# Performance work log

Hardware: AMD Instinct MI355X
Metric: run time of the kernel (lower is better)

Reference implementation:

```python
import jax, jax.numpy as jnp
import numpy as np

B, Cin, Cout, H, W = 8, 64, 128, 64, 64
DI, N, R, K = 256, 16, 8, 4  # d_inner, d_state, dt_rank, scan directions
EPS = 1e-5


def setup_inputs() -> dict:
    key = jax.random.key(0)
    ks = jax.random.split(key, 12)
    rn = lambda k, s, sc=1.0: jax.random.normal(k, s, jnp.float32) * sc
    inp = {
        "x": rn(ks[0], (B, Cin, H, W)),
        "conv1_w": rn(ks[1], (Cout, Cin, 3, 3), 0.05),
        "bn1_g": jnp.ones((Cout,)), "bn1_b": jnp.zeros((Cout,)),
        "bn1_m": jnp.zeros((Cout,)), "bn1_v": jnp.ones((Cout,)),
        "conv2_w": rn(ks[2], (Cout, Cout, 3, 3), 0.05),
        "bn2_g": jnp.ones((Cout,)), "bn2_b": jnp.zeros((Cout,)),
        "bn2_m": jnp.zeros((Cout,)), "bn2_v": jnp.ones((Cout,)),
        "ln_g": jnp.ones((Cout,)), "ln_b": jnp.zeros((Cout,)),
        "in_proj_w": rn(ks[3], (2 * DI, Cout), 0.05),
        "in_proj_b": jnp.zeros((2 * DI,)),
        "dw_w": rn(ks[4], (DI, 1, 3, 3), 0.2),
        "dw_b": jnp.zeros((DI,)),
        "x_proj_w": rn(ks[5], (K, R + 2 * N, DI), 0.05),
        "dt_proj_w": rn(ks[6], (K, DI, R), 0.1),
        "dt_proj_b": rn(ks[7], (K, DI), 0.1),
        "A_log": jnp.log(jnp.broadcast_to(jnp.arange(1, N + 1, dtype=jnp.float32), (K, DI, N))),
        "Ds": jnp.ones((K, DI)),
        "out_norm_g": jnp.ones((DI,)), "out_norm_b": jnp.zeros((DI,)),
        "out_proj_w": rn(ks[8], (Cout, DI), 0.05),
        "out_proj_b": jnp.zeros((Cout,)),
    }
    return inp


def _conv(x, w, groups=1):
    return jax.lax.conv_general_dilated(x, w, (1, 1), 'SAME',
        dimension_numbers=('NCHW', 'OIHW', 'NCHW'), feature_group_count=groups)


def _bn(x, g, b, m, v):
    inv = g / jnp.sqrt(v + EPS)
    return x * inv[:, None, None] + (b - m * inv)[:, None, None]


def _ln_cf(x, g, b):
    # LayerNorm over channel axis, channel-first [B,C,H,W]
    mu = x.mean(1, keepdims=True)
    var = ((x - mu) ** 2).mean(1, keepdims=True)
    return (x - mu) / jnp.sqrt(var + EPS) * g[None, :, None, None] + b[None, :, None, None]


def _selective_scan(u, dt, A, Bs, Cs, Ds):
    # u, dt: [B,K,D,L]; Bs, Cs: [B,K,N,L]; A: [K,D,N]; Ds: [K,D]
    uT = jnp.moveaxis(u, -1, 0)    # [L,B,K,D]
    dtT = jnp.moveaxis(dt, -1, 0)  # [L,B,K,D]
    BT = jnp.moveaxis(Bs, -1, 0)   # [L,B,K,N]
    CT = jnp.moveaxis(Cs, -1, 0)   # [L,B,K,N]

    def step(h, inp):
        u_i, dt_i, B_i, C_i = inp
        dA = jnp.exp(dt_i[..., None] * A)                       # [B,K,D,N]
        h = dA * h + (dt_i * u_i)[..., None] * B_i[:, :, None, :]
        y = jnp.einsum('bkdn,bkn->bkd', h, C_i)
        return h, y

    h0 = jnp.zeros(u.shape[:3] + (A.shape[-1],), u.dtype)       # [B,K,D,N]
    _, ys = jax.lax.scan(step, h0, (uT, dtT, BT, CT))
    ys = jnp.moveaxis(ys, 0, -1)                                # [B,K,D,L]
    return ys + u * Ds[None, :, :, None]


def _ss2d(x, ln_g, ln_b, in_proj_w, in_proj_b, dw_w, dw_b, x_proj_w,
          dt_proj_w, dt_proj_b, A_log, Ds, out_norm_g, out_norm_b,
          out_proj_w, out_proj_b):
    b, c, h, w = x.shape
    L = h * w
    xn = _ln_cf(x, ln_g, ln_b)
    xz = jnp.einsum('bchw,oc->bohw', xn, in_proj_w) + in_proj_b[None, :, None, None]
    xg, z = xz[:, :DI], xz[:, DI:]
    xc = jax.nn.silu(_conv(xg, dw_w, groups=DI) + dw_b[None, :, None, None])  # [B,DI,H,W]

    # cross-scan: 4 traversal orders of the 2D grid
    x_hw = xc.reshape(b, DI, L)
    x_wh = xc.transpose(0, 1, 3, 2).reshape(b, DI, L)
    xs = jnp.stack([x_hw, x_wh, jnp.flip(x_hw, -1), jnp.flip(x_wh, -1)], 1)  # [B,K,DI,L]

    x_dbl = jnp.einsum('bkdl,kcd->bkcl', xs, x_proj_w)
    dts, Bs, Cs = x_dbl[:, :, :R], x_dbl[:, :, R:R + N], x_dbl[:, :, R + N:]
    dt = jax.nn.softplus(jnp.einsum('bkrl,kdr->bkdl', dts, dt_proj_w)
                         + dt_proj_b[None, :, :, None])
    A = -jnp.exp(A_log)

    ys = _selective_scan(xs, dt, A, Bs, Cs, Ds)                 # [B,K,DI,L]

    # cross-merge: undo each traversal and sum
    y_wh = ys[:, 1] + jnp.flip(ys[:, 3], -1)
    y = ys[:, 0] + jnp.flip(ys[:, 2], -1) \
        + y_wh.reshape(b, DI, w, h).transpose(0, 1, 3, 2).reshape(b, DI, L)
    y = y.reshape(b, DI, h, w)

    y = _ln_cf(y, out_norm_g, out_norm_b)
    y = y * jax.nn.silu(z)
    return jnp.einsum('bdhw,od->bohw', y, out_proj_w) + out_proj_b[None, :, None, None]


def reference(x, conv1_w, bn1_g, bn1_b, bn1_m, bn1_v, conv2_w, bn2_g, bn2_b,
              bn2_m, bn2_v, ln_g, ln_b, in_proj_w, in_proj_b, dw_w, dw_b,
              x_proj_w, dt_proj_w, dt_proj_b, A_log, Ds, out_norm_g,
              out_norm_b, out_proj_w, out_proj_b):
    # CNN stem: conv-BN-ReLU x2 (eval mode; Dropout2d identity)
    hcnn = jax.nn.relu(_bn(_conv(x, conv1_w), bn1_g, bn1_b, bn1_m, bn1_v))
    hcnn = jax.nn.relu(_bn(_conv(hcnn, conv2_w), bn2_g, bn2_b, bn2_m, bn2_v))
    # VSSBlock: residual + SS2D(LN(x))
    out = hcnn + _ss2d(hcnn, ln_g, ln_b, in_proj_w, in_proj_b, dw_w, dw_b,
                       x_proj_w, dt_proj_w, dt_proj_b, A_log, Ds,
                       out_norm_g, out_norm_b, out_proj_w, out_proj_b)
    return out
```

## Files before the change

### kernel.cpp

```cpp
#include <hip/hip_runtime.h>
#include <hip/hip_bf16.h>
#include <math.h>

typedef __hip_bfloat16 bf16;
typedef float f32x4 __attribute__((ext_vector_type(4)));
typedef float f32x2 __attribute__((ext_vector_type(2)));
typedef short s8v   __attribute__((ext_vector_type(8)));

#define EPSV 1e-5f
#define C1c  64
#define C2c  128
#define Ls   4096
#define DIc  256
#define NCH  64
#define CHL  64
#define LOG2E 1.44269504f

#define CPAD 40
#define SM_CONVM_BYTES ((3*66*CPAD + 9*64*CPAD)*2)
#define SM_PROJ2_BYTES ((192*CPAD + 64*CPAD)*2)
#define SM_SCAN   (32*40)
#define SM_NORM_BYTES (64*266*2 + 512*4)
#define SM_OUT_BYTES  ((64*CPAD + 128*CPAD)*2)

template<bool BF>
__device__ __forceinline__ float LD(const void* p, size_t i){
  if constexpr(BF) return __bfloat162float(((const bf16*)p)[i]);
  else return ((const float*)p)[i];
}

__device__ __forceinline__ int smap(int k, int l){
  if(k==0) return l;
  if(k==1) return ((l&63)<<6) | (l>>6);
  if(k==2) return 4095 - l;
  int lp = 4095 - l; return ((lp&63)<<6) | (lp>>6);
}

__device__ __forceinline__ float* sbase(float* S1, float* S2, int bid){
  return (bid & 1024) ? (S2 + ((size_t)(bid & 1023) << 12))
                      : (S1 + ((size_t)bid << 12));
}

__global__ void k_flag(const unsigned int* __restrict__ g1, int* __restrict__ fl){
  if(threadIdx.x==0 && blockIdx.x==0) *fl = (g1[0]==0x3F800000u) ? 0 : 1;
}

template<bool BF>
__device__ void wprep_impl(const void* w1, const void* w2, const void* w3, const void* w4s,
    const void* w5s, bf16* W1P, bf16* W2P, bf16* W3P, bf16* W4P, bf16* W5P){
  int idx = blockIdx.x*256 + threadIdx.x;
  if(idx < 9*128*64){
    int kk = idx>>13; int rem = idx&8191; int co = rem>>6; int ci = rem&63;
    W1P[idx] = __float2bfloat16(LD<BF>(w1, ((size_t)co*64+ci)*9 + kk));
  } else if(idx < 9*128*64 + 9*128*128){
    int i2 = idx - 9*128*64;
    int kk = i2>>14; int rem = i2&16383; int co = rem>>7; int ci = rem&127;
    W2P[i2] = __float2bfloat16(LD<BF>(w2, ((size_t)co*128+ci)*9 + kk));
  } else if(idx < 9*128*64 + 9*128*128 + 128*256){
    int i3 = idx - (9*128*64 + 9*128*128);
    W3P[i3] = __float2bfloat16(LD<BF>(w3, i3));
  } else if(idx < 9*128*64 + 9*128*128 + 128*256 + 512*128){
    int i4 = idx - (9*128*64 + 9*128*128 + 128*256);
    W4P[i4] = __float2bfloat16(LD<BF>(w4s, i4));
  } else if(idx < 9*128*64 + 9*128*128 + 128*256 + 512*128 + 4*48*256){
    int i5 = idx - (9*128*64 + 9*128*128 + 128*256 + 512*128);
    int k5 = i5/12288; int rem = i5 - k5*12288;
    int m = rem>>8; int c = rem&255;
    float v = (m < 40) ? LD<BF>(w5s, ((size_t)(k5*40+m))*256 + c) : 0.f;
    W5P[i5] = __float2bfloat16(v);
  }
}
__global__ __launch_bounds__(256) void k_wprep(const int* fl, const void* w1, const void* w2,
    const void* w3, const void* w4s, const void* w5s,
    bf16* W1P, bf16* W2P, bf16* W3P, bf16* W4P, bf16* W5P){
  if(*fl) wprep_impl<true>(w1,w2,w3,w4s,w5s,W1P,W2P,W3P,W4P,W5P);
  else    wprep_impl<false>(w1,w2,w3,w4s,w5s,W1P,W2P,W3P,W4P,W5P);
}

template<bool BF>
__device__ void xprep_impl(float* tile, const void* x, bf16* XT){
  int bid = blockIdx.x; int sc = bid & 63; int b = bid>>6;
  int t = threadIdx.x;
  #pragma unroll
  for(int i=0;i<16;i++){
    int flat = t + 256*i;
    int ci = flat>>6, px = flat&63;
    tile[ci*65+px] = LD<BF>(x, ((size_t)b*64+ci)*Ls + sc*64 + px);
  }
  __syncthreads();
  #pragma unroll
  for(int i=0;i<16;i++){
    int flat = t + 256*i;
    int px = flat>>6, ci = flat&63;
    XT[((size_t)b*Ls + sc*64 + px)*64 + ci] = __float2bfloat16(tile[ci*65+px]);
  }
}
__global__ __launch_bounds__(256) void k_xprep(const int* fl, const void* x, bf16* XT){
  __shared__ float tile[64*65];
  if(*fl) xprep_impl<true>(tile,x,XT); else xprep_impl<false>(tile,x,XT);
}

template<bool BFW, int CIN, bool OUTCL>
__device__ void convm2_impl(bf16* smb, const bf16* __restrict__ xt, const bf16* __restrict__ wp,
    const void* __restrict__ gg, const void* __restrict__ bbp, const void* __restrict__ mm,
    const void* __restrict__ vv, void* __restrict__ out){
  bf16* bx = smb;
  bf16* wl = smb + 3*66*CPAD;
  int bid = blockIdx.x;
  int y = bid & 63; int cog = (bid>>6)&1; int b = bid>>7;
  int t = threadIdx.x;
  int w = t>>6; int lane = t&63; int n = lane&15; int q = lane>>4;

  for(int i=t; i<3*66*CPAD/2; i+=256) ((unsigned int*)bx)[i] = 0u;

  f32x4 acc[4];
  #pragma unroll
  for(int pt=0;pt<4;pt++) acc[pt] = (f32x4){0.f,0.f,0.f,0.f};

  for(int ci0=0; ci0<CIN; ci0+=32){
    __syncthreads();
    #pragma unroll
    for(int i=0;i<3;i++){
      int idx = t + 256*i;
      int c8 = idx&3, px = (idx>>2)&63, r = idx>>8;
      int gy = y + r - 1;
      if((unsigned)gy < 64u){
        uint4 v = *(const uint4*)(xt + ((size_t)b*Ls + (gy<<6) + px)*CIN + ci0 + c8*8);
        *(uint4*)(bx + ((r*66) + px+1)*CPAD + c8*8) = v;
      }
    }
    #pragma unroll
    for(int i=0;i<9;i++){
      int idx = t + 256*i;
      int c8 = idx&3, co = (idx>>2)&63, kk = idx>>8;
      uint4 v = *(const uint4*)(wp + ((size_t)kk*128 + cog*64+co)*CIN + ci0 + c8*8);
      *(uint4*)(wl + (kk*64+co)*CPAD + c8*8) = v;
    }
    __syncthreads();
    #pragma unroll
    for(int kk=0; kk<9; kk++){
      int ky = kk/3, kx = kk - ky*3;
      s8v A = *(const s8v*)(wl + (kk*64 + w*16 + n)*CPAD + q*8);
      #pragma unroll
      for(int pt=0;pt<4;pt++){
        s8v B = *(const s8v*)(bx + (ky*66 + pt*16 + n + kx)*CPAD + q*8);
        acc[pt] = __builtin_amdgcn_mfma_f32_16x16x32_bf16(A, B, acc[pt], 0, 0, 0);
      }
    }
  }
  float inv[4], bias[4];
  #pragma unroll
  for(int i=0;i<4;i++){
    int co = cog*64 + w*16 + q*4 + i;
    float iv = LD<BFW>(gg,co)/sqrtf(LD<BFW>(vv,co)+EPSV);
    inv[i] = iv;
    bias[i] = LD<BFW>(bbp,co) - LD<BFW>(mm,co)*iv;
  }
  #pragma unroll
  for(int pt=0;pt<4;pt++){
    int px = pt*16 + n;
    if constexpr(OUTCL){
      ushort4 o4;
      unsigned short* ov = (unsigned short*)&o4;
      #pragma unroll
      for(int i=0;i<4;i++){
        float v = acc[pt][i]*inv[i] + bias[i];
        v = v>0.f ? v : 0.f;
        bf16 bv = __float2bfloat16(v);
        ov[i] = *(unsigned short*)&bv;
      }
      *(ushort4*)((bf16*)out + ((size_t)b*Ls + (y<<6) + px)*128 + cog*64 + w*16 + q*4) = o4;
    } else {
      #pragma unroll
      for(int i=0;i<4;i++){
        int co = cog*64 + w*16 + q*4 + i;
        float v = acc[pt][i]*inv[i] + bias[i];
        ((float*)out)[((size_t)b*C2c + co)*Ls + (y<<6) + px] = v>0.f ? v : 0.f;
      }
    }
  }
}
__global__ __launch_bounds__(256) void k_conv1(const int* fl, const bf16* xt, const bf16* wp,
    const void* g, const void* bb, const void* mm, const void* vv, bf16* out){
  extern __shared__ float sm[];
  bf16* smb = (bf16*)sm;
  if(*fl) convm2_impl<true ,C1c,true>(smb,xt,wp,g,bb,mm,vv,out);
  else    convm2_impl<false,C1c,true>(smb,xt,wp,g,bb,mm,vv,out);
}
__global__ __launch_bounds__(256) void k_conv2(const int* fl, const bf16* xt, const bf16* wp,
    const void* g, const void* bb, const void* mm, const void* vv, float* out){
  extern __shared__ float sm[];
  bf16* smb = (bf16*)sm;
  if(*fl) convm2_impl<true ,C2c,false>(smb,xt,wp,g,bb,mm,vv,out);
  else    convm2_impl<false,C2c,false>(smb,xt,wp,g,bb,mm,vv,out);
}

template<bool BF>
__device__ void ln1_impl(const float* __restrict__ hc, const void* __restrict__ g,
    const void* __restrict__ bb, float* __restrict__ xn){
  int t = threadIdx.x;
  int pos = blockIdx.x*64 + (t>>2);
  int part = t&3;
  int b = pos >> 12; int s = pos & 4095;
  const float* base = hc + (size_t)b*C2c*Ls + (size_t)(part*32)*Ls + s;
  float v[32];
  float sum=0.f, sq=0.f;
  #pragma unroll
  for(int j=0;j<32;j++){
    float x = base[(size_t)j*Ls];
    v[j] = x; sum += x; sq += x*x;
  }
  sum += __shfl_xor(sum,1); sum += __shfl_xor(sum,2);
  sq  += __shfl_xor(sq,1);  sq  += __shfl_xor(sq,2);
  float mu  = sum*(1.f/C2c);
  float var = sq*(1.f/C2c) - mu*mu;
  float inv = rsqrtf(var + EPSV);
  float* ob = xn + (size_t)b*C2c*Ls + (size_t)(part*32)*Ls + s;
  #pragma unroll
  for(int j=0;j<32;j++){
    int c = part*32 + j;
    ob[(size_t)j*Ls] = (v[j]-mu)*inv*LD<BF>(g,c) + LD<BF>(bb,c);
  }
}
__global__ __launch_bounds__(256) void k_ln1(const int* fl, const float* hc, const void* g,
    const void* bb, float* xn){
  if(*fl) ln1_impl<true>(hc,g,bb,xn); else ln1_impl<false>(hc,g,bb,xn);
}

template<bool BF>
__device__ void inprojm_impl(bf16* smb, const float* __restrict__ xn, const bf16* __restrict__ w4,
    const void* __restrict__ ipb, float* __restrict__ xg, float* __restrict__ sz){
  bf16* bm = smb;
  bf16* wl = smb + 64*CPAD;
  int bid = blockIdx.x;
  int y = bid & 63; int og = (bid>>6)&3; int b = bid>>8;
  int t = threadIdx.x;
  int w = t>>6; int lane = t&63; int n = lane&15; int q = lane>>4;
  f32x4 acc[2][4];
  #pragma unroll
  for(int si=0;si<2;si++)
    #pragma unroll
    for(int pt=0;pt<4;pt++) acc[si][pt] = (f32x4){0.f,0.f,0.f,0.f};
  for(int c0=0; c0<C2c; c0+=32){
    __syncthreads();
    #pragma unroll
    for(int i=0;i<2;i++){
      int task = t + 256*i;
      int px = task & 63; int cq = task >> 6;
      const float* src = xn + ((size_t)(b*C2c + c0 + cq*4))*Ls + (y<<6) + px;
      ushort4 o4;
      unsigned short* ov = (unsigned short*)&o4;
      #pragma unroll
      for(int r=0;r<4;r++){
        bf16 bv = __float2bfloat16(src[(size_t)r*Ls]);
        ov[r] = *(unsigned short*)&bv;
      }
      *(ushort4*)(bm + px*CPAD + cq*4) = o4;
    }
    #pragma unroll
    for(int i=0;i<2;i++){
      int idx = t + 256*i;
      int co = idx>>2, c8 = idx&3;
      *(uint4*)(wl + co*CPAD + c8*8) = *(const uint4*)(w4 + (size_t)(og*128+co)*C2c + c0 + c8*8);
    }
    __syncthreads();
    #pragma unroll
    for(int si=0;si<2;si++){
      s8v A = *(const s8v*)(wl + ((w*2+si)*16 + n)*CPAD + q*8);
      #pragma unroll
      for(int pt=0;pt<4;pt++){
        s8v B = *(const s8v*)(bm + (pt*16+n)*CPAD + q*8);
        acc[si][pt] = __builtin_amdgcn_mfma_f32_16x16x32_bf16(A, B, acc[si][pt], 0, 0, 0);
      }
    }
  }
  #pragma unroll
  for(int si=0;si<2;si++){
    #pragma unroll
    for(int i=0;i<4;i++){
      int o = og*128 + (w*2+si)*16 + q*4 + i;
      float bias = LD<BF>(ipb, o);
      #pragma unroll
      for(int pt=0;pt<4;pt++){
        int px = pt*16 + n;
        float v = acc[si][pt][i] + bias;
        size_t off = ((size_t)b*DIc + (o & 255))*Ls + (y<<6) + px;
        if(o < 256) xg[off] = v;
        else        sz[off] = v/(1.f+__expf(-v));
      }
    }
  }
}
__global__ __launch_bounds__(256) void k_inproj(const int* fl, const float* xn, const bf16* w4,
    const void* ipb, float* xg, float* sz){
  extern __shared__ float sm[];
  bf16* smb = (bf16*)sm;
  if(*fl) inprojm_impl<true>(smb,xn,w4,ipb,xg,sz); else inprojm_impl<false>(smb,xn,w4,ipb,xg,sz);
}

template<bool BF>
__device__ void dwconv_impl(const float* __restrict__ xg, const void* __restrict__ wt,
    const void* __restrict__ bias, float* __restrict__ xc){
  int bid = blockIdx.x;
  int st = bid & 15; int d = (bid>>4)&255; int b = bid>>12;
  int s = st*256 + threadIdx.x;
  int h = s>>6, w = s&63;
  const float* base = xg + ((size_t)b*DIc + d)*Ls;
  float acc = LD<BF>(bias, d);
  #pragma unroll
  for(int kh=0;kh<3;kh++){
    int hh = h+kh-1;
    if((unsigned)hh<64u){
      #pragma unroll
      for(int kw=0;kw<3;kw++){
        int ww = w+kw-1;
        if((unsigned)ww<64u) acc += base[(hh<<6)+ww]*LD<BF>(wt, d*9+kh*3+kw);
      }
    }
  }
  xc[((size_t)b*DIc+d)*Ls + s] = acc/(1.f+__expf(-acc));
}
__global__ __launch_bounds__(256) void k_dwconv(const int* fl, const float* xg, const void* wt,
    const void* bias, float* xc){
  if(*fl) dwconv_impl<true>(xg,wt,bias,xc); else dwconv_impl<false>(xg,wt,bias,xc);
}

__global__ __launch_bounds__(256) void k_trans(const float* __restrict__ xc, float* __restrict__ xcT){
  __shared__ float tile[64*65];
  int bid = blockIdx.x; int sc = bid & 63; int dc = (bid>>6)&3; int b = bid>>8;
  int s0 = sc*64, d0 = dc*64;
  int t = threadIdx.x;
  #pragma unroll
  for(int i=0;i<16;i++){
    int flat = t + 256*i;
    int dd = flat>>6, ss = flat&63;
    tile[dd*65+ss] = xc[((size_t)b*DIc + d0+dd)*Ls + s0+ss];
  }
  __syncthreads();
  #pragma unroll
  for(int i=0;i<16;i++){
    int flat = t + 256*i;
    int ss = flat>>6, dd = flat&63;
    xcT[((size_t)b*Ls + s0+ss)*DIc + d0+dd] = tile[dd*65+ss];
  }
}

__global__ __launch_bounds__(256) void k_proj2(const float* __restrict__ xcT,
    const bf16* __restrict__ w5, float* __restrict__ proj){
  extern __shared__ float smf[];
  bf16* wl = (bf16*)smf;
  bf16* bm = wl + 192*CPAD;
  int bid = blockIdx.x;
  int y = bid & 63; int b = bid>>6;
  int s0 = y*64;
  int t = threadIdx.x;
  int w = t>>6; int lane = t&63; int n = lane&15; int q = lane>>4;
  f32x4 acc[3][4];
  #pragma unroll
  for(int si=0;si<3;si++)
    #pragma unroll
    for(int pt=0;pt<4;pt++) acc[si][pt] = (f32x4){0.f,0.f,0.f,0.f};
  for(int c0=0; c0<DIc; c0+=32){
    __syncthreads();
    #pragma unroll
    for(int i=0;i<3;i++){
      int idx = t + 256*i;
      int co = idx>>2, c8 = idx&3;
      *(uint4*)(wl + co*CPAD + c8*8) = *(const uint4*)(w5 + (size_t)co*DIc + c0 + c8*8);
    }
    {
      int px = t & 63; int cq = t >> 6;
      const float* src = xcT + ((size_t)b*Ls + s0 + px)*DIc + c0 + cq*8;
      float4 v0 = *(const float4*)(src);
      float4 v1 = *(const float4*)(src+4);
      ushort4 o0, o1;
      unsigned short* p0 = (unsigned short*)&o0;
      unsigned short* p1 = (unsigned short*)&o1;
      const float* pv0 = (const float*)&v0;
      const float* pv1 = (const float*)&v1;
      #pragma unroll
      for(int r=0;r<4;r++){
        bf16 b0 = __float2bfloat16(pv0[r]); p0[r] = *(unsigned short*)&b0;
        bf16 b1 = __float2bfloat16(pv1[r]); p1[r] = *(unsigned short*)&b1;
      }
      *(ushort4*)(bm + px*CPAD + cq*8)     = o0;
      *(ushort4*)(bm + px*CPAD + cq*8 + 4) = o1;
    }
    __syncthreads();
    #pragma unroll
    for(int si=0;si<3;si++){
      s8v A = *(const s8v*)(wl + (w*48 + si*16 + n)*CPAD + q*8);
      #pragma unroll
      for(int pt=0;pt<4;pt++){
        s8v B = *(const s8v*)(bm + (pt*16+n)*CPAD + q*8);
        acc[si][pt] = __builtin_amdgcn_mfma_f32_16x16x32_bf16(A, B, acc[si][pt], 0, 0, 0);
      }
    }
  }
  float* ob = proj + (((size_t)b*4 + w)*Ls + s0)*40;
  #pragma unroll
  for(int si=0;si<3;si++){
    if(si==2 && q>=2) continue;
    int m0 = si*16 + q*4;
    #pragma unroll
    for(int pt=0;pt<4;pt++){
      int px = pt*16 + n;
      float4 v4; v4.x=acc[si][pt][0]; v4.y=acc[si][pt][1]; v4.z=acc[si][pt][2]; v4.w=acc[si][pt][3];
      *(float4*)(ob + (size_t)px*40 + m0) = v4;
    }
  }
}

template<bool BF>
__device__ void scanA_impl(float* lp, const float* __restrict__ xcT, const float* __restrict__ proj,
    const void* __restrict__ dtw_g, const void* __restrict__ dtb_g, const void* __restrict__ alog,
    float* __restrict__ SDT, float* __restrict__ S1, float* __restrict__ S2){
  int bid = blockIdx.x; int c = bid&63; int k = (bid>>6)&3; int b = bid>>8;
  int d = threadIdx.x;
  alignas(16) f32x2 dtw2[4];
  #pragma unroll
  for(int r=0;r<8;r++) ((float*)dtw2)[r] = LD<BF>(dtw_g, (k*DIc+d)*8 + r);
  float dtb = LD<BF>(dtb_g, k*DIc+d);
  const size_t abase = (size_t)(k*DIc+d)*16;
  alignas(16) f32x2 h2[8];
  #pragma unroll
  for(int m=0;m<8;m++) h2[m] = (f32x2){0.f,0.f};
  bool il = true;
  #pragma unroll
  for(int n=0;n<16;n++){
    float e = __expf(LD<BF>(alog, abase+n));
    il = il && (fabsf(e - (float)(n+1)) < 0.03f*(n+1));
  }
  il = __all(il);
  float sum_dt = 0.f;
  const float* xb = xcT + (size_t)b*Ls*DIc + d;
  const float* pjb = proj + (((size_t)b*4 + k)*Ls)*40;
  int l0 = c*CHL;
  for(int gq=0; gq<2; gq++){
    int lb = l0 + gq*32;
    __syncthreads();
    {
      int f4 = threadIdx.x;
      int j = f4/10, r4 = f4-j*10;
      int s = smap(k, lb+j);
      ((float4*)lp)[f4] = *(const float4*)(pjb + (size_t)s*40 + r4*4);
      f4 += 256;
      if(f4 < 320){
        int j2 = f4/10, r42 = f4-j2*10;
        int s2 = smap(k, lb+j2);
        ((float4*)lp)[f4] = *(const float4*)(pjb + (size_t)s2*40 + r42*4);
      }
    }
    __syncthreads();
    if(il){
      for(int j=0;j<32;j++){
        int s = smap(k, lb+j);
        float u = xb[(size_t)s*DIc];
        const float* row = lp + j*40;
        alignas(16) f32x2 dv2[4];
        alignas(16) f32x2 bv2[8];
        *(float4*)&dv2[0] = *(const float4*)(row);
        *(float4*)&dv2[2] = *(const float4*)(row+4);
        *(float4*)&bv2[0] = *(const float4*)(row+8);
        *(float4*)&bv2[2] = *(const float4*)(row+12);
        *(float4*)&bv2[4] = *(const float4*)(row+16);
        *(float4*)&bv2[6] = *(const float4*)(row+20);
        f32x2 xd2 = (f32x2){dtb, 0.f};
        #pragma unroll
        for(int m=0;m<4;m++) xd2 = xd2 + dv2[m]*dtw2[m];
        float xdt = xd2.x + xd2.y;
        float dt = fmaxf(xdt,0.f) + __logf(1.f+__expf(-fabsf(xdt)));
        sum_dt += dt;
        float du = dt*u;
        float e1 = exp2f(-dt*LOG2E);
        float e2 = e1*e1;
        f32x2 p2  = (f32x2){e1, e2};
        f32x2 e22 = (f32x2){e2, e2};
        f32x2 du2 = (f32x2){du, du};
        #pragma unroll
        for(int m=0;m<8;m++){
          h2[m] = p2*h2[m] + du2*bv2[m];
          p2 = p2*e22;
        }
      }
    } else {
      for(int j=0;j<32;j++){
        int s = smap(k, lb+j);
        float u = xb[(size_t)s*DIc];
        const float* row = lp + j*40;
        float dv[8], bv[16];
        *(float4*)&dv[0] = *(const float4*)(row);
        *(float4*)&dv[4] = *(const float4*)(row+4);
        *(float4*)&bv[0]  = *(const float4*)(row+8);
        *(float4*)&bv[4]  = *(const float4*)(row+12);
        *(float4*)&bv[8]  = *(const float4*)(row+16);
        *(float4*)&bv[12] = *(const float4*)(row+20);
        float xdt = dtb;
        #pragma unroll
        for(int r=0;r<8;r++) xdt += dv[r]*((float*)dtw2)[r];
        float dt = fmaxf(xdt,0.f) + __logf(1.f+__expf(-fabsf(xdt)));
        sum_dt += dt;
        float du = dt*u;
        float* hs = (float*)h2;
        #pragma unroll
        for(int n=0;n<16;n++){
          float a = __expf(LD<BF>(alog, abase+n));
          float dA = exp2f(-dt*a*LOG2E);
          hs[n] = dA*hs[n] + du*bv[n];
        }
      }
    }
  }
  float* Sb = sbase(S1, S2, bid) + (d<<4);
  #pragma unroll
  for(int m=0;m<4;m++) *(float4*)(Sb + 4*m) = *(float4*)&h2[2*m];
  SDT[((size_t)bid<<8) + d] = sum_dt;
}
__global__ __launch_bounds__(256) void k_scanA(const int* fl, const float* xcT, const float* proj,
    const void* dtw, const void* dtb, const void* alog, float* SDT, float* S1, float* S2){
  extern __shared__ float sm[];
  if(*fl) scanA_impl<true>(sm,xcT,proj,dtw,dtb,alog,SDT,S1,S2);
  else    scanA_impl<false>(sm,xcT,proj,dtw,dtb,alog,SDT,S1,S2);
}

template<bool BF>
__device__ void scanB_impl(const void* __restrict__ alog, const float* __restrict__ SDT,
    float* __restrict__ S1, float* __restrict__ S2){
  int tid = blockIdx.x*256 + threadIdx.x;
  int bk = tid >> 12; int rem = tid & 4095;
  int k = bk & 3; int d = rem >> 4; int n = rem & 15;
  float e = __expf(LD<BF>(alog, ((size_t)(k*DIc+d)<<4) + n));
  float h = 0.f;
  for(int c=0;c<NCH;c++){
    int bid = (bk<<6) + c;
    float* base = sbase(S1, S2, bid);
    float p = exp2f(-e*LOG2E*SDT[((size_t)bid<<8) + d]);
    float s = base[rem];
    base[rem] = h;
    h = p*h + s;
  }
}
__global__ __launch_bounds__(256) void k_scanB(const int* fl, const void* alog,
    const float* SDT, float* S1, float* S2){
  if(*fl) scanB_impl<true>(alog,SDT,S1,S2); else scanB_impl<false>(alog,SDT,S1,S2);
}

template<bool BF>
__device__ void scanC_impl(float* lp, const float* __restrict__ xcT, const float* __restrict__ proj,
    const void* __restrict__ dtw_g, const void* __restrict__ dtb_g, const void* __restrict__ alog,
    const void* __restrict__ ds_g, float* __restrict__ S1, float* __restrict__ S2,
    float* __restrict__ Y){
  int bid = blockIdx.x; int c = bid&63; int k = (bid>>6)&3; int b = bid>>8;
  int d = threadIdx.x;
  alignas(16) f32x2 dtw2[4];
  #pragma unroll
  for(int r=0;r<8;r++) ((float*)dtw2)[r] = LD<BF>(dtw_g, (k*DIc+d)*8 + r);
  float dtb = LD<BF>(dtb_g, k*DIc+d);
  float Dsv = LD<BF>(ds_g, k*DIc+d);
  const size_t abase = (size_t)(k*DIc+d)*16;
  const float* hin = sbase(S1, S2, bid) + (d<<4);
  alignas(16) f32x2 h2[8];
  #pragma unroll
  for(int m=0;m<4;m++) *(float4*)&h2[2*m] = *(const float4*)(hin + 4*m);
  bool il = true;
  #pragma unroll
  for(int n=0;n<16;n++){
    float e = __expf(LD<BF>(alog, abase+n));
    il = il && (fabsf(e - (float)(n+1)) < 0.03f*(n+1));
  }
  il = __all(il);
  const float* xb = xcT + (size_t)b*Ls*DIc + d;
  const float* pjb = proj + (((size_t)b*4 + k)*Ls)*40;
  float* Yb = Y + (size_t)b*Ls*DIc + d;
  int l0 = c*CHL;
  for(int gq=0; gq<2; gq++){
    int lb = l0 + gq*32;
    __syncthreads();
    {
      int f4 = threadIdx.x;
      int j = f4/10, r4 = f4-j*10;
      int s = smap(k, lb+j);
      ((float4*)lp)[f4] = *(const float4*)(pjb + (size_t)s*40 + r4*4);
      f4 += 256;
      if(f4 < 320){
        int j2 = f4/10, r42 = f4-j2*10;
        int s2 = smap(k, lb+j2);
        ((float4*)lp)[f4] = *(const float4*)(pjb + (size_t)s2*40 + r42*4);
      }
    }
    __syncthreads();
    if(il){
      for(int j=0;j<32;j++){
        int s = smap(k, lb+j);
        float u = xb[(size_t)s*DIc];
        const float* row = lp + j*40;
        alignas(16) f32x2 dv2[4];
        alignas(16) f32x2 bv2[8], cv2[8];
        *(float4*)&dv2[0] = *(const float4*)(row);
        *(float4*)&dv2[2] = *(const float4*)(row+4);
        *(float4*)&bv2[0] = *(const float4*)(row+8);
        *(float4*)&bv2[2] = *(const float4*)(row+12);
        *(float4*)&bv2[4] = *(const float4*)(row+16);
        *(float4*)&bv2[6] = *(const float4*)(row+20);
        *(float4*)&cv2[0] = *(const float4*)(row+24);
        *(float4*)&cv2[2] = *(const float4*)(row+28);
        *(float4*)&cv2[4] = *(const float4*)(row+32);
        *(float4*)&cv2[6] = *(const float4*)(row+36);
        f32x2 xd2 = (f32x2){dtb, 0.f};
        #pragma unroll
        for(int m=0;m<4;m++) xd2 = xd2 + dv2[m]*dtw2[m];
        float xdt = xd2.x + xd2.y;
        float dt = fmaxf(xdt,0.f) + __logf(1.f+__expf(-fabsf(xdt)));
        float du = dt*u;
        float e1 = exp2f(-dt*LOG2E);
        float e2 = e1*e1;
        f32x2 p2  = (f32x2){e1, e2};
        f32x2 e22 = (f32x2){e2, e2};
        f32x2 du2 = (f32x2){du, du};
        f32x2 y2  = (f32x2){0.f, 0.f};
        #pragma unroll
        for(int m=0;m<8;m++){
          h2[m] = p2*h2[m] + du2*bv2[m];
          y2 = y2 + h2[m]*cv2[m];
          p2 = p2*e22;
        }
        float y = y2.x + y2.y;
        atomicAdd(Yb + (size_t)s*DIc, y + u*Dsv);
      }
    } else {
      for(int j=0;j<32;j++){
        int s = smap(k, lb+j);
        float u = xb[(size_t)s*DIc];
        const float* row = lp + j*40;
        float dv[8], bv[16], cv[16];
        *(float4*)&dv[0] = *(const float4*)(row);
        *(float4*)&dv[4] = *(const float4*)(row+4);
        *(float4*)&bv[0]  = *(const float4*)(row+8);
        *(float4*)&bv[4]  = *(const float4*)(row+12);
        *(float4*)&bv[8]  = *(const float4*)(row+16);
        *(float4*)&bv[12] = *(const float4*)(row+20);
        *(float4*)&cv[0]  = *(const float4*)(row+24);
        *(float4*)&cv[4]  = *(const float4*)(row+28);
        *(float4*)&cv[8]  = *(const float4*)(row+32);
        *(float4*)&cv[12] = *(const float4*)(row+36);
        float xdt = dtb;
        #pragma unroll
        for(int r=0;r<8;r++) xdt += dv[r]*((float*)dtw2)[r];
        float dt = fmaxf(xdt,0.f) + __logf(1.f+__expf(-fabsf(xdt)));
        float du = dt*u;
        float y = 0.f;
        float* hs = (float*)h2;
        #pragma unroll
        for(int n=0;n<16;n++){
          float a = __expf(LD<BF>(alog, abase+n));
          float dA = exp2f(-dt*a*LOG2E);
          hs[n] = dA*hs[n] + du*bv[n];
          y += hs[n]*cv[n];
        }
        atomicAdd(Yb + (size_t)s*DIc, y + u*Dsv);
      }
    }
  }
}
__global__ __launch_bounds__(256) void k_scanC(const int* fl, const float* xcT, const float* proj,
    const void* dtw, const void* dtb, const void* alog, const void* ds,
    float* S1, float* S2, float* Y){
  extern __shared__ float sm[];
  if(*fl) scanC_impl<true>(sm,xcT,proj,dtw,dtb,alog,ds,S1,S2,Y);
  else    scanC_impl<false>(sm,xcT,proj,dtw,dtb,alog,ds,S1,S2,Y);
}

template<bool BF>
__device__ void norm_impl(float* sm, const float* __restrict__ Y, const float* __restrict__ sz,
    const void* __restrict__ ong, const void* __restrict__ onb, bf16* __restrict__ M){
  bf16*  szT = (bf16*)sm;
  float* gg  = sm + (64*266)/2;
  float* bb2 = gg + 256;
  int bid = blockIdx.x; int sc = bid & 63; int b = bid>>6; int s0 = sc*64;
  int t = threadIdx.x;
  int px = t>>2, q = t&3;
  gg[t]  = LD<BF>(ong, t);
  bb2[t] = LD<BF>(onb, t);
  #pragma unroll
  for(int i=0;i<64;i++){
    int flat = t + 256*i;
    int d2 = flat>>6, p2 = flat&63;
    szT[p2*266 + d2] = __float2bfloat16(sz[((size_t)b*DIc + d2)*Ls + s0 + p2]);
  }
  const float* yb = Y + ((size_t)b*Ls + s0 + px)*256 + q*64;
  float4 va[16];
  float sum=0.f, sq=0.f;
  #pragma unroll
  for(int i=0;i<16;i++){
    float4 v = *(const float4*)(yb + 4*i);
    va[i] = v;
    sum += v.x+v.y+v.z+v.w;
    sq  += v.x*v.x+v.y*v.y+v.z*v.z+v.w*v.w;
  }
  sum += __shfl_xor(sum,1); sum += __shfl_xor(sum,2);
  sq  += __shfl_xor(sq,1);  sq  += __shfl_xor(sq,2);
  float mu  = sum*(1.f/256.f);
  float var = sq*(1.f/256.f) - mu*mu;
  float inv = rsqrtf(var + EPSV);
  __syncthreads();
  bf16* mb = M + ((size_t)b*Ls + s0 + px)*256 + q*64;
  #pragma unroll
  for(int i=0;i<16;i++){
    float4 v = va[i];
    float* pv = (float*)&v;
    ushort4 o4;
    unsigned short* ov = (unsigned short*)&o4;
    #pragma unroll
    for(int j=0;j<4;j++){
      int d2 = q*64 + 4*i + j;
      float m = ((pv[j]-mu)*inv*gg[d2] + bb2[d2]) * __bfloat162float(szT[px*266 + d2]);
      bf16 bm = __float2bfloat16(m);
      ov[j] = *(unsigned short*)&bm;
    }
    *(ushort4*)(mb + 4*i) = o4;
  }
}
__global__ __launch_bounds__(256) void k_norm(const int* fl, const float* Y, const float* sz,
    const void* ong, const void* onb, bf16* M){
  extern __shared__ float sm[];
  if(*fl) norm_impl<true>(sm,Y,sz,ong,onb,M); else norm_impl<false>(sm,Y,sz,ong,onb,M);
}

template<bool BF>
__device__ void outp_impl(bf16* smb, const bf16* __restrict__ M, const bf16* __restrict__ w3,
    const void* __restrict__ opb, const float* __restrict__ hc, void* __restrict__ out){
  bf16* bm = smb;
  bf16* wl = smb + 64*CPAD;
  int bid = blockIdx.x;
  int y = bid & 63; int b = bid>>6;
  int t = threadIdx.x;
  int w = t>>6; int lane = t&63; int n = lane&15; int q = lane>>4;
  f32x4 acc[2][4];
  #pragma unroll
  for(int si=0;si<2;si++)
    #pragma unroll
    for(int pt=0;pt<4;pt++) acc[si][pt] = (f32x4){0.f,0.f,0.f,0.f};
  for(int d0=0; d0<256; d0+=32){
    __syncthreads();
    {
      int pxs = t>>2, c8 = t&3;
      *(uint4*)(bm + pxs*CPAD + c8*8) = *(const uint4*)(M + ((size_t)b*Ls + (y<<6) + pxs)*256 + d0 + c8*8);
    }
    #pragma unroll
    for(int i=0;i<2;i++){
      int idx = t + 256*i;
      int co = idx>>2, c8 = idx&3;
      *(uint4*)(wl + co*CPAD + c8*8) = *(const uint4*)(w3 + (size_t)co*256 + d0 + c8*8);
    }
    __syncthreads();
    #pragma unroll
    for(int si=0;si<2;si++){
      s8v A = *(const s8v*)(wl + ((w*2+si)*16 + n)*CPAD + q*8);
      #pragma unroll
      for(int pt=0;pt<4;pt++){
        s8v B = *(const s8v*)(bm + (pt*16+n)*CPAD + q*8);
        acc[si][pt] = __builtin_amdgcn_mfma_f32_16x16x32_bf16(A, B, acc[si][pt], 0, 0, 0);
      }
    }
  }
  #pragma unroll
  for(int si=0;si<2;si++){
    #pragma unroll
    for(int i=0;i<4;i++){
      int co = (w*2+si)*16 + q*4 + i;
      float bias = LD<BF>(opb, co);
      const float* hb = hc + ((size_t)b*C2c + co)*Ls + (y<<6);
      #pragma unroll
      for(int pt=0;pt<4;pt++){
        int px = pt*16 + n;
        float v = acc[si][pt][i] + bias + hb[px];
        size_t off = ((size_t)b*C2c + co)*Ls + (y<<6) + px;
        if constexpr(BF) ((bf16*)out)[off] = __float2bfloat16(v);
        else ((float*)out)[off] = v;
      }
    }
  }
}
__global__ __launch_bounds__(256) void k_out(const int* fl, const bf16* M, const bf16* w3,
    const void* opb, const float* hc, void* out){
  extern __shared__ float sm[];
  bf16* smb = (bf16*)sm;
  if(*fl) outp_impl<true>(smb,M,w3,opb,hc,out); else outp_impl<false>(smb,M,w3,opb,hc,out);
}

extern "C" void kernel_launch(void* const* d_in, const int* in_sizes, int n_in,
                              void* d_out, int out_size, void* d_ws, size_t ws_size,
                              hipStream_t stream){
  const void* x        = d_in[0];
  const void* conv1_w  = d_in[1];
  const void* bn1_g    = d_in[2];
  const void* bn1_b    = d_in[3];
  const void* bn1_m    = d_in[4];
  const void* bn1_v    = d_in[5];
  const void* conv2_w  = d_in[6];
  const void* bn2_g    = d_in[7];
  const void* bn2_b    = d_in[8];
  const void* bn2_m    = d_in[9];
  const void* bn2_v    = d_in[10];
  const void* ln_g     = d_in[11];
  const void* ln_b     = d_in[12];
  const void* in_proj_w= d_in[13];
  const void* in_proj_b= d_in[14];
  const void* dw_w     = d_in[15];
  const void* dw_b     = d_in[16];
  const void* x_proj_w = d_in[17];
  const void* dt_proj_w= d_in[18];
  const void* dt_proj_b= d_in[19];
  const void* A_log    = d_in[20];
  const void* Ds       = d_in[21];
  const void* out_norm_g=d_in[22];
  const void* out_norm_b=d_in[23];
  const void* out_proj_w=d_in[24];
  const void* out_proj_b=d_in[25];

  float* w = (float*)d_ws;
  float* A1   = w;
  float* HC   = w + 4194304;
  float* XG   = w + 8388608;
  float* SZ   = w + 16777216;
  float* XC   = w + 25165824;
  float* PROJ = w + 33554432;
  float* Sbuf = w + 38797312;
  int*   FLAG = (int*)(w + 42991616);
  bf16*  W3P  = (bf16*)(w + 42991620);
  bf16*  W4P  = W3P + 32768;
  bf16*  W5P  = W4P + 65536;
  float* XCT  = XG;
  float* Y    = XC;
  float* SDT  = XC;
  float* S1   = Sbuf;
  float* S2   = A1;
  bf16*  H1T  = (bf16*)A1;
  bf16*  XT   = (bf16*)XC;
  bf16*  W1P  = (bf16*)PROJ;
  bf16*  W2P  = W1P + 9*128*64;
  bf16*  M    = (bf16*)XG;

  k_flag  <<<1,64,0,stream>>>((const unsigned int*)bn1_g, FLAG);
  k_wprep <<< 1440,256,0,stream>>>(FLAG, conv1_w, conv2_w, out_proj_w, in_proj_w, x_proj_w,
                                   W1P, W2P, W3P, W4P, W5P);
  k_xprep <<<  512,256,0,stream>>>(FLAG, x, XT);
  k_conv1 <<< 1024,256,SM_CONVM_BYTES,stream>>>(FLAG, XT, W1P, bn1_g, bn1_b, bn1_m, bn1_v, H1T);
  k_conv2 <<< 1024,256,SM_CONVM_BYTES,stream>>>(FLAG, H1T, W2P, bn2_g, bn2_b, bn2_m, bn2_v, HC);
  k_ln1   <<<  512,256,0,stream>>>(FLAG, HC, ln_g, ln_b, A1);
  k_inproj<<< 2048,256,SM_OUT_BYTES,stream>>>(FLAG, A1, W4P, in_proj_b, XG, SZ);
  k_dwconv<<<32768,256,0,stream>>>(FLAG, XG, dw_w, dw_b, XC);
  k_trans <<< 2048,256,0,stream>>>(XC, XCT);
  k_proj2 <<<  512,256,SM_PROJ2_BYTES,stream>>>(XCT, W5P, PROJ);
  k_scanA <<< 2048,256,SM_SCAN*4,stream>>>(FLAG, XCT, PROJ, dt_proj_w, dt_proj_b, A_log, SDT, S1, S2);
  k_scanB <<<  512,256,0,stream>>>(FLAG, A_log, SDT, S1, S2);
  (void)hipMemsetAsync(Y, 0, (size_t)8388608*4, stream);
  k_scanC <<< 2048,256,SM_SCAN*4,stream>>>(FLAG, XCT, PROJ, dt_proj_w, dt_proj_b, A_log, Ds, S1, S2, Y);
  k_norm  <<<  512,256,SM_NORM_BYTES,stream>>>(FLAG, Y, SZ, out_norm_g, out_norm_b, M);
  k_out   <<<  512,256,SM_OUT_BYTES,stream>>>(FLAG, M, W3P, out_proj_b, HC, d_out);
}
```

Before: 521.3 us.

## Fuse LayerNorm into in_proj load and depthwise conv into transpose

Replaces the standalone LayerNorm kernel with a stats-only kernel that stores per-position mean and inverse std. The in_proj kernel now normalizes the conv2 output on the fly while staging it into shared memory. The depthwise conv plus SiLU is merged with the layout transpose, writing the transposed result directly. This removes two full-size intermediate tensor round trips and a launch, at the cost of recomputing the normalization per output-channel group and reshuffled workspace aliasing.

```diff
diff --git a/kernel.cpp b/kernel.cpp
--- a/kernel.cpp
+++ b/kernel.cpp
@@ -22,6 +22,7 @@
 #define SM_SCAN   (32*40)
 #define SM_NORM_BYTES (64*266*2 + 512*4)
 #define SM_OUT_BYTES  ((64*CPAD + 128*CPAD)*2)
+#define SM_INPROJ_BYTES ((64*CPAD + 128*CPAD)*2 + 384*4)
 
 template<bool BF>
 __device__ __forceinline__ float LD(const void* p, size_t i){
@@ -195,47 +196,51 @@
   else    convm2_impl<false,C2c,false>(smb,xt,wp,g,bb,mm,vv,out);
 }
 
-template<bool BF>
-__device__ void ln1_impl(const float* __restrict__ hc, const void* __restrict__ g,
-    const void* __restrict__ bb, float* __restrict__ xn){
+__global__ __launch_bounds__(256) void k_stats(const float* __restrict__ hc,
+    float* __restrict__ stats){
   int t = threadIdx.x;
   int pos = blockIdx.x*64 + (t>>2);
   int part = t&3;
   int b = pos >> 12; int s = pos & 4095;
   const float* base = hc + (size_t)b*C2c*Ls + (size_t)(part*32)*Ls + s;
-  float v[32];
   float sum=0.f, sq=0.f;
   #pragma unroll
   for(int j=0;j<32;j++){
     float x = base[(size_t)j*Ls];
-    v[j] = x; sum += x; sq += x*x;
+    sum += x; sq += x*x;
   }
   sum += __shfl_xor(sum,1); sum += __shfl_xor(sum,2);
   sq  += __shfl_xor(sq,1);  sq  += __shfl_xor(sq,2);
-  float mu  = sum*(1.f/C2c);
-  float var = sq*(1.f/C2c) - mu*mu;
-  float inv = rsqrtf(var + EPSV);
-  float* ob = xn + (size_t)b*C2c*Ls + (size_t)(part*32)*Ls + s;
-  #pragma unroll
-  for(int j=0;j<32;j++){
-    int c = part*32 + j;
-    ob[(size_t)j*Ls] = (v[j]-mu)*inv*LD<BF>(g,c) + LD<BF>(bb,c);
-  }
-}
-__global__ __launch_bounds__(256) void k_ln1(const int* fl, const float* hc, const void* g,
-    const void* bb, float* xn){
-  if(*fl) ln1_impl<true>(hc,g,bb,xn); else ln1_impl<false>(hc,g,bb,xn);
-}
-
-template<bool BF>
-__device__ void inprojm_impl(bf16* smb, const float* __restrict__ xn, const bf16* __restrict__ w4,
-    const void* __restrict__ ipb, float* __restrict__ xg, float* __restrict__ sz){
+  if(part==0){
+    float mu  = sum*(1.f/C2c);
+    float var = sq*(1.f/C2c) - mu*mu;
+    stats[pos]         = mu;
+    stats[32768 + pos] = rsqrtf(var + EPSV);
+  }
+}
+
+template<bool BF>
+__device__ void inprojm_impl(bf16* smb, const float* __restrict__ hc,
+    const float* __restrict__ stats, const void* __restrict__ lng, const void* __restrict__ lnb,
+    const bf16* __restrict__ w4, const void* __restrict__ ipb,
+    float* __restrict__ xg, float* __restrict__ sz){
   bf16* bm = smb;
   bf16* wl = smb + 64*CPAD;
+  float* gg  = (float*)(smb + 64*CPAD + 128*CPAD);
+  float* bb2 = gg + 128;
+  float* muv = bb2 + 128;
+  float* ivv = muv + 64;
   int bid = blockIdx.x;
   int y = bid & 63; int og = (bid>>6)&3; int b = bid>>8;
   int t = threadIdx.x;
   int w = t>>6; int lane = t&63; int n = lane&15; int q = lane>>4;
+  if(t < 128){ gg[t] = LD<BF>(lng, t); bb2[t] = LD<BF>(lnb, t); }
+  else if(t < 192){
+    int px = t - 128;
+    int pos = b*4096 + y*64 + px;
+    muv[px] = stats[pos];
+    ivv[px] = stats[32768 + pos];
+  }
   f32x4 acc[2][4];
   #pragma unroll
   for(int si=0;si<2;si++)
@@ -247,12 +252,15 @@
     for(int i=0;i<2;i++){
       int task = t + 256*i;
       int px = task & 63; int cq = task >> 6;
-      const float* src = xn + ((size_t)(b*C2c + c0 + cq*4))*Ls + (y<<6) + px;
+      const float* src = hc + ((size_t)(b*C2c + c0 + cq*4))*Ls + (y<<6) + px;
+      float mu = muv[px], iv = ivv[px];
       ushort4 o4;
       unsigned short* ov = (unsigned short*)&o4;
       #pragma unroll
       for(int r=0;r<4;r++){
-        bf16 bv = __float2bfloat16(src[(size_t)r*Ls]);
+        int c = c0 + cq*4 + r;
+        float vn = (src[(size_t)r*Ls] - mu)*iv*gg[c] + bb2[c];
+        bf16 bv = __float2bfloat16(vn);
         ov[r] = *(unsigned short*)&bv;
       }
       *(ushort4*)(bm + px*CPAD + cq*4) = o4;
@@ -291,58 +299,52 @@
     }
   }
 }
-__global__ __launch_bounds__(256) void k_inproj(const int* fl, const float* xn, const bf16* w4,
-    const void* ipb, float* xg, float* sz){
+__global__ __launch_bounds__(256) void k_inproj(const int* fl, const float* hc, const float* stats,
+    const void* lng, const void* lnb, const bf16* w4, const void* ipb, float* xg, float* sz){
   extern __shared__ float sm[];
   bf16* smb = (bf16*)sm;
-  if(*fl) inprojm_impl<true>(smb,xn,w4,ipb,xg,sz); else inprojm_impl<false>(smb,xn,w4,ipb,xg,sz);
-}
-
-template<bool BF>
-__device__ void dwconv_impl(const float* __restrict__ xg, const void* __restrict__ wt,
-    const void* __restrict__ bias, float* __restrict__ xc){
+  if(*fl) inprojm_impl<true>(smb,hc,stats,lng,lnb,w4,ipb,xg,sz);
+  else    inprojm_impl<false>(smb,hc,stats,lng,lnb,w4,ipb,xg,sz);
+}
+
+template<bool BF>
+__device__ void dwt_impl(float* tile, const float* __restrict__ xg, const void* __restrict__ wt,
+    const void* __restrict__ bias, float* __restrict__ xcT){
   int bid = blockIdx.x;
-  int st = bid & 15; int d = (bid>>4)&255; int b = bid>>12;
-  int s = st*256 + threadIdx.x;
-  int h = s>>6, w = s&63;
-  const float* base = xg + ((size_t)b*DIc + d)*Ls;
-  float acc = LD<BF>(bias, d);
-  #pragma unroll
-  for(int kh=0;kh<3;kh++){
-    int hh = h+kh-1;
-    if((unsigned)hh<64u){
-      #pragma unroll
-      for(int kw=0;kw<3;kw++){
-        int ww = w+kw-1;
-        if((unsigned)ww<64u) acc += base[(hh<<6)+ww]*LD<BF>(wt, d*9+kh*3+kw);
-      }
-    }
-  }
-  xc[((size_t)b*DIc+d)*Ls + s] = acc/(1.f+__expf(-acc));
-}
-__global__ __launch_bounds__(256) void k_dwconv(const int* fl, const float* xg, const void* wt,
-    const void* bias, float* xc){
-  if(*fl) dwconv_impl<true>(xg,wt,bias,xc); else dwconv_impl<false>(xg,wt,bias,xc);
-}
-
-__global__ __launch_bounds__(256) void k_trans(const float* __restrict__ xc, float* __restrict__ xcT){
-  __shared__ float tile[64*65];
-  int bid = blockIdx.x; int sc = bid & 63; int dc = (bid>>6)&3; int b = bid>>8;
-  int s0 = sc*64, d0 = dc*64;
+  int h = bid & 63; int dc = (bid>>6)&3; int b = bid>>8;
   int t = threadIdx.x;
   #pragma unroll
   for(int i=0;i<16;i++){
     int flat = t + 256*i;
-    int dd = flat>>6, ss = flat&63;
-    tile[dd*65+ss] = xc[((size_t)b*DIc + d0+dd)*Ls + s0+ss];
+    int dl = flat>>6; int ww = flat&63;
+    int d = dc*64 + dl;
+    const float* base = xg + ((size_t)(b*DIc + d))*Ls;
+    float acc = LD<BF>(bias, d);
+    #pragma unroll
+    for(int kh=0;kh<3;kh++){
+      int hh = h+kh-1;
+      if((unsigned)hh<64u){
+        #pragma unroll
+        for(int kw=0;kw<3;kw++){
+          int w2 = ww+kw-1;
+          if((unsigned)w2<64u) acc += base[(hh<<6)+w2]*LD<BF>(wt, d*9+kh*3+kw);
+        }
+      }
+    }
+    tile[dl*65+ww] = acc/(1.f+__expf(-acc));
   }
   __syncthreads();
   #pragma unroll
   for(int i=0;i<16;i++){
     int flat = t + 256*i;
-    int ss = flat>>6, dd = flat&63;
-    xcT[((size_t)b*Ls + s0+ss)*DIc + d0+dd] = tile[dd*65+ss];
-  }
+    int w2 = flat>>6; int dl = flat&63;
+    xcT[((size_t)b*Ls + (h<<6) + w2)*DIc + dc*64 + dl] = tile[dl*65+w2];
+  }
+}
+__global__ __launch_bounds__(256) void k_dwt(const int* fl, const float* xg, const void* wt,
+    const void* bias, float* xcT){
+  __shared__ float tile[64*65];
+  if(*fl) dwt_impl<true>(tile,xg,wt,bias,xcT); else dwt_impl<false>(tile,xg,wt,bias,xcT);
 }
 
 __global__ __launch_bounds__(256) void k_proj2(const float* __restrict__ xcT,
@@ -830,16 +832,17 @@
   bf16*  W3P  = (bf16*)(w + 42991620);
   bf16*  W4P  = W3P + 32768;
   bf16*  W5P  = W4P + 65536;
-  float* XCT  = XG;
-  float* Y    = XC;
-  float* SDT  = XC;
+  float* STATS= A1;
+  float* XCT  = XC;
+  float* Y    = XG;
+  float* SDT  = XG;
   float* S1   = Sbuf;
   float* S2   = A1;
   bf16*  H1T  = (bf16*)A1;
   bf16*  XT   = (bf16*)XC;
   bf16*  W1P  = (bf16*)PROJ;
   bf16*  W2P  = W1P + 9*128*64;
-  bf16*  M    = (bf16*)XG;
+  bf16*  M    = (bf16*)A1;
 
   k_flag  <<<1,64,0,stream>>>((const unsigned int*)bn1_g, FLAG);
   k_wprep <<< 1440,256,0,stream>>>(FLAG, conv1_w, conv2_w, out_proj_w, in_proj_w, x_proj_w,
@@ -847,10 +850,9 @@
   k_xprep <<<  512,256,0,stream>>>(FLAG, x, XT);
   k_conv1 <<< 1024,256,SM_CONVM_BYTES,stream>>>(FLAG, XT, W1P, bn1_g, bn1_b, bn1_m, bn1_v, H1T);
   k_conv2 <<< 1024,256,SM_CONVM_BYTES,stream>>>(FLAG, H1T, W2P, bn2_g, bn2_b, bn2_m, bn2_v, HC);
-  k_ln1   <<<  512,256,0,stream>>>(FLAG, HC, ln_g, ln_b, A1);
-  k_inproj<<< 2048,256,SM_OUT_BYTES,stream>>>(FLAG, A1, W4P, in_proj_b, XG, SZ);
-  k_dwconv<<<32768,256,0,stream>>>(FLAG, XG, dw_w, dw_b, XC);
-  k_trans <<< 2048,256,0,stream>>>(XC, XCT);
+  k_stats <<<  512,256,0,stream>>>(HC, STATS);
+  k_inproj<<< 2048,256,SM_INPROJ_BYTES,stream>>>(FLAG, HC, STATS, ln_g, ln_b, W4P, in_proj_b, XG, SZ);
+  k_dwt   <<< 2048,256,0,stream>>>(FLAG, XG, dw_w, dw_b, XCT);
   k_proj2 <<<  512,256,SM_PROJ2_BYTES,stream>>>(XCT, W5P, PROJ);
   k_scanA <<< 2048,256,SM_SCAN*4,stream>>>(FLAG, XCT, PROJ, dt_proj_w, dt_proj_b, A_log, SDT, S1, S2);
   k_scanB <<<  512,256,0,stream>>>(FLAG, A_log, SDT, S1, S2);
```

Result: faster. 505.1 us (-3.1%).
